# Optimization experiments

Hardware: AMD Instinct MI355X
Metric: run time of the kernel (lower is better)

The kernel has to match this reference:

```python
import jax, jax.numpy as jnp
import numpy as np

N_NODES = 100000
N_REL = 3
N_EDGES = 300000
IN_FEAT = 256
OUT_FEAT = 256


def setup_inputs() -> dict:
    key = jax.random.key(0)
    k1, k2, k3, k4 = jax.random.split(key, 4)
    x = jax.random.normal(k1, (N_NODES, IN_FEAT), dtype=jnp.float32)
    weight = jax.random.normal(k2, (N_REL, IN_FEAT, OUT_FEAT), dtype=jnp.float32)
    src = jax.random.randint(k3, (N_REL, N_EDGES), 0, N_NODES, dtype=jnp.int64)
    dst = jax.random.randint(k4, (N_REL, N_EDGES), 0, N_NODES, dtype=jnp.int64)
    return {"x": x, "weight": weight, "src": src, "dst": dst}


def reference(x, weight, src, dst):
    # Per-relation dense transform: h[r] = x @ W[r]   -> [R, N, out]
    h = jnp.einsum('ni,rio->rno', x, weight)
    n_nodes = x.shape[0]

    # Sparse unweighted-sum aggregation per relation (adj @ h), accumulated
    # into a single destination-node buffer (single node type).
    def agg_one(h_r, src_r, dst_r):
        msgs = h_r[src_r]  # gather source features [E, out]
        return jax.ops.segment_sum(msgs, dst_r, num_segments=n_nodes)

    per_rel = jax.vmap(agg_one)(h, src, dst)  # [R, N, out]
    return jax.nn.relu(per_rel.sum(axis=0))
```

## Files before the change

### kernel.cpp

```cpp
#include <hip/hip_runtime.h>
#include <hip/hip_bf16.h>
#include <stdint.h>

#define M_NODES 100000
#define KF 256
#define NF 256
#define NRELS 3
#define NEDGES 300000
#define TOT_EDGES (NRELS * NEDGES)
#define TOTK (NRELS * M_NODES)
#define KCAT (NRELS * KF)
#define BM 64
#define PAD8 8
#define OVF_SLOTS 16
#define XELEM (M_NODES * KF)
#define EB ((TOT_EDGES + 255) / 256)
#define XCONV_BLOCKS (XELEM / 8 / 256)
#define WT_BLOCKS ((NF * KCAT + 255) / 256)

typedef __attribute__((ext_vector_type(8))) short bf16x8;
typedef __attribute__((ext_vector_type(8))) unsigned short u16x8;
typedef __attribute__((ext_vector_type(4))) float f32x4;

__device__ __forceinline__ unsigned short f32_to_bf16(float f) {
    union { float f; uint32_t u; } c; c.f = f;
    uint32_t u = c.u;
    uint32_t r = (u + 0x7FFFu + ((u >> 16) & 1u)) >> 16;
    return (unsigned short)r;
}

__device__ __forceinline__ float bf16_to_f32(unsigned short s) {
    union { uint32_t u; float f; } c; c.u = ((uint32_t)s) << 16;
    return c.f;
}

__global__ __launch_bounds__(256)
void k_build(const float* __restrict__ x, const float* __restrict__ w,
             const int* __restrict__ src, const int* __restrict__ dst,
             unsigned short* __restrict__ xb, unsigned short* __restrict__ Bt,
             int* __restrict__ counts, int* __restrict__ perm8,
             int* __restrict__ ovf)
{
    int b = blockIdx.x;
    if (b < EB) {
        int e = b * 256 + threadIdx.x;
        if (e < TOT_EDGES) {
            int r = e / NEDGES;
            int key = r * M_NODES + dst[e];
            int pos = atomicAdd(&counts[key], 1);
            if (pos < PAD8)
                perm8[(size_t)key * PAD8 + pos] = src[e];
            else if (pos < PAD8 + OVF_SLOTS)
                ovf[(size_t)key * OVF_SLOTS + (pos - PAD8)] = src[e];
        }
    } else if (b < EB + XCONV_BLOCKS) {
        int gid = (b - EB) * 256 + threadIdx.x;
        const float4* p = (const float4*)x + (size_t)gid * 2;
        float4 u = p[0], v = p[1];
        u16x8 o;
        o[0] = f32_to_bf16(u.x); o[1] = f32_to_bf16(u.y);
        o[2] = f32_to_bf16(u.z); o[3] = f32_to_bf16(u.w);
        o[4] = f32_to_bf16(v.x); o[5] = f32_to_bf16(v.y);
        o[6] = f32_to_bf16(v.z); o[7] = f32_to_bf16(v.w);
        *(u16x8*)(xb + (size_t)gid * 8) = o;
    } else {
        int gid = (b - EB - XCONV_BLOCKS) * 256 + threadIdx.x;
        if (gid < NF * KCAT) {
            int n = gid / KCAT;
            int kc = gid - n * KCAT;
            int r = kc >> 8, k = kc & 255;
            Bt[(size_t)n * KCAT + kc] = f32_to_bf16(w[((size_t)r * KF + k) * NF + n]);
        }
    }
}

__global__ __launch_bounds__(512, 4)
void gemm_ga(const unsigned short* __restrict__ xb,
             const unsigned short* __restrict__ Bt,
             const int* __restrict__ cnt, const int* __restrict__ perm8,
             const int* __restrict__ ovf,
             float* __restrict__ out)
{
    const int d0 = blockIdx.x * BM;
    const int t = threadIdx.x;
    const int lane = t & 63;
    const int wv = t >> 6;
    const int l16 = lane & 15, lg = lane >> 4;
    const int hw = t >> 5;
    const int hl = t & 31;

    __shared__ short As[BM * 256];

    f32x4 acc[4][2] = {};
    const u16x8 zz = (u16x8)0;

    int oc0 = 0, oc1 = 0, oc2 = 0;
    if (hl < 4) {
        int kb = d0 + hw * 4 + hl;
        if (kb >= M_NODES) kb = M_NODES - 1;
        oc0 = cnt[kb];
        oc1 = cnt[M_NODES + kb];
        oc2 = cnt[2 * M_NODES + kb];
    }

    int kpre = d0 + hw * 4 + (hl >> 3);
    if (kpre >= M_NODES) kpre = M_NODES - 1;

    for (int r = 0; r < NRELS; ++r) {
        int ocr = (r == 0) ? oc0 : ((r == 1) ? oc1 : oc2);

        int pv = perm8[((size_t)(r * M_NODES + kpre)) * PAD8 + (hl & 7)];

        if (r) __syncthreads();

#pragma unroll
        for (int q = 0; q < 4; ++q) {
            int n = __shfl(ocr, q, 32);
            if (n > PAD8 + OVF_SLOTS) n = PAD8 + OVF_SLOTS;
            float a0=0.f,a1=0.f,a2=0.f,a3=0.f,a4=0.f,a5=0.f,a6=0.f,a7=0.f;

            auto acc4 = [&](int s0, int s1, int s2, int s3,
                            bool c1, bool c2, bool c3) {
                u16x8 v0 = *(const u16x8*)(xb + (size_t)s0 * KF + hl * 8);
                u16x8 v1 = c1 ? *(const u16x8*)(xb + (size_t)s1 * KF + hl * 8) : zz;
                u16x8 v2 = c2 ? *(const u16x8*)(xb + (size_t)s2 * KF + hl * 8) : zz;
                u16x8 v3 = c3 ? *(const u16x8*)(xb + (size_t)s3 * KF + hl * 8) : zz;
                a0 += bf16_to_f32(v0[0]) + bf16_to_f32(v1[0]) + bf16_to_f32(v2[0]) + bf16_to_f32(v3[0]);
                a1 += bf16_to_f32(v0[1]) + bf16_to_f32(v1[1]) + bf16_to_f32(v2[1]) + bf16_to_f32(v3[1]);
                a2 += bf16_to_f32(v0[2]) + bf16_to_f32(v1[2]) + bf16_to_f32(v2[2]) + bf16_to_f32(v3[2]);
                a3 += bf16_to_f32(v0[3]) + bf16_to_f32(v1[3]) + bf16_to_f32(v2[3]) + bf16_to_f32(v3[3]);
                a4 += bf16_to_f32(v0[4]) + bf16_to_f32(v1[4]) + bf16_to_f32(v2[4]) + bf16_to_f32(v3[4]);
                a5 += bf16_to_f32(v0[5]) + bf16_to_f32(v1[5]) + bf16_to_f32(v2[5]) + bf16_to_f32(v3[5]);
                a6 += bf16_to_f32(v0[6]) + bf16_to_f32(v1[6]) + bf16_to_f32(v2[6]) + bf16_to_f32(v3[6]);
                a7 += bf16_to_f32(v0[7]) + bf16_to_f32(v1[7]) + bf16_to_f32(v2[7]) + bf16_to_f32(v3[7]);
            };

            if (n > 0)
                acc4(__shfl(pv, q * 8 + 0, 32), __shfl(pv, q * 8 + 1, 32),
                     __shfl(pv, q * 8 + 2, 32), __shfl(pv, q * 8 + 3, 32),
                     1 < n, 2 < n, 3 < n);
            if (n > 4)
                acc4(__shfl(pv, q * 8 + 4, 32), __shfl(pv, q * 8 + 5, 32),
                     __shfl(pv, q * 8 + 6, 32), __shfl(pv, q * 8 + 7, 32),
                     5 < n, 6 < n, 7 < n);
            if (n > 8) {
                int kq = d0 + hw * 4 + q;
                if (kq >= M_NODES) kq = M_NODES - 1;
                int ex = (hl < n - 8)
                    ? ovf[((size_t)(r * M_NODES + kq)) * OVF_SLOTS + hl] : 0;
                for (int j = 8; j < n; j += 4) {
                    int s0 = __shfl(ex, j - 8 + 0, 32);
                    int s1 = __shfl(ex, j - 8 + 1, 32);
                    int s2 = __shfl(ex, j - 8 + 2, 32);
                    int s3 = __shfl(ex, j - 8 + 3, 32);
                    acc4(s0, s1, s2, s3, j + 1 < n, j + 2 < n, j + 3 < n);
                }
            }

            int row = hw * 4 + q;
            u16x8 o;
            o[0] = f32_to_bf16(a0); o[1] = f32_to_bf16(a1);
            o[2] = f32_to_bf16(a2); o[3] = f32_to_bf16(a3);
            o[4] = f32_to_bf16(a4); o[5] = f32_to_bf16(a5);
            o[6] = f32_to_bf16(a6); o[7] = f32_to_bf16(a7);
            int slot = hl ^ (row & 7);
            *(u16x8*)((char*)As + row * 512 + slot * 16) = o;
        }
        __syncthreads();

        const unsigned short* bb = Bt + (size_t)(wv * 32 + l16) * KCAT
                                      + r * 256 + lg * 8;
#pragma unroll
        for (int kt = 0; kt < 8; ++kt) {
            bf16x8 bfr[2];
#pragma unroll
            for (int j = 0; j < 2; ++j)
                bfr[j] = *(const bf16x8*)(bb + (size_t)j * 16 * KCAT + kt * 32);
            bf16x8 afr[4];
#pragma unroll
            for (int i = 0; i < 4; ++i) {
                int arow = i * 16 + l16;
                int slot = (kt * 4 + lg) ^ (arow & 7);
                afr[i] = *(bf16x8*)((char*)As + arow * 512 + slot * 16);
            }
#pragma unroll
            for (int i = 0; i < 4; ++i)
#pragma unroll
                for (int j = 0; j < 2; ++j)
                    acc[i][j] = __builtin_amdgcn_mfma_f32_16x16x32_bf16(
                        afr[i], bfr[j], acc[i][j], 0, 0, 0);
        }
    }

#pragma unroll
    for (int i = 0; i < 4; ++i) {
        int row_base = d0 + i * 16 + lg * 4;
#pragma unroll
        for (int q = 0; q < 4; ++q) {
            int row = row_base + q;
            if (row < M_NODES) {
#pragma unroll
                for (int j = 0; j < 2; ++j) {
                    int col = wv * 32 + j * 16 + l16;
                    out[(size_t)row * NF + col] = fmaxf(acc[i][j][q], 0.f);
                }
            }
        }
    }
}

extern "C" void kernel_launch(void* const* d_in, const int* in_sizes, int n_in,
                              void* d_out, int out_size, void* d_ws, size_t ws_size,
                              hipStream_t stream)
{
    const float* x   = (const float*)d_in[0];
    const float* w   = (const float*)d_in[1];
    const int*   src = (const int*)d_in[2];
    const int*   dst = (const int*)d_in[3];
    float* out = (float*)d_out;

    char* ws = (char*)d_ws;
    size_t o = 0;
    int* counts = (int*)(ws + o);  o += (size_t)TOTK * 4;
    int* perm8  = (int*)(ws + o);  o += (size_t)TOTK * PAD8 * 4;
    int* ovf    = (int*)(ws + o);  o += (size_t)TOTK * OVF_SLOTS * 4;
    unsigned short* Bt = (unsigned short*)(ws + o); o += (size_t)NF * KCAT * 2;
    unsigned short* xb = (unsigned short*)(ws + o); o += (size_t)XELEM * 2;

    hipMemsetAsync(counts, 0, (size_t)TOTK * 4, stream);

    k_build<<<EB + XCONV_BLOCKS + WT_BLOCKS, 256, 0, stream>>>(
        x, w, src, dst, xb, Bt, counts, perm8, ovf);

    gemm_ga<<<(M_NODES + BM - 1) / BM, 512, 0, stream>>>(
        xb, Bt, counts, perm8, ovf, out);
}
```

Before: 215.1 us.

## Software-pipeline neighbor gathers across rows and hoist loads above barrier

```diff
diff --git a/kernel.cpp b/kernel.cpp
--- a/kernel.cpp
+++ b/kernel.cpp
@@ -32,6 +32,11 @@
 __device__ __forceinline__ float bf16_to_f32(unsigned short s) {
     union { uint32_t u; float f; } c; c.u = ((uint32_t)s) << 16;
     return c.f;
+}
+
+__device__ __forceinline__ void bar_lgkm() {
+    asm volatile("s_waitcnt lgkmcnt(0)" ::: "memory");
+    __builtin_amdgcn_s_barrier();
 }
 
 __global__ __launch_bounds__(256)
@@ -111,62 +116,77 @@
 
         int pv = perm8[((size_t)(r * M_NODES + kpre)) * PAD8 + (hl & 7)];
 
-        if (r) __syncthreads();
-
-#pragma unroll
-        for (int q = 0; q < 4; ++q) {
-            int n = __shfl(ocr, q, 32);
-            if (n > PAD8 + OVF_SLOTS) n = PAD8 + OVF_SLOTS;
-            float a0=0.f,a1=0.f,a2=0.f,a3=0.f,a4=0.f,a5=0.f,a6=0.f,a7=0.f;
-
-            auto acc4 = [&](int s0, int s1, int s2, int s3,
-                            bool c1, bool c2, bool c3) {
-                u16x8 v0 = *(const u16x8*)(xb + (size_t)s0 * KF + hl * 8);
-                u16x8 v1 = c1 ? *(const u16x8*)(xb + (size_t)s1 * KF + hl * 8) : zz;
-                u16x8 v2 = c2 ? *(const u16x8*)(xb + (size_t)s2 * KF + hl * 8) : zz;
-                u16x8 v3 = c3 ? *(const u16x8*)(xb + (size_t)s3 * KF + hl * 8) : zz;
-                a0 += bf16_to_f32(v0[0]) + bf16_to_f32(v1[0]) + bf16_to_f32(v2[0]) + bf16_to_f32(v3[0]);
-                a1 += bf16_to_f32(v0[1]) + bf16_to_f32(v1[1]) + bf16_to_f32(v2[1]) + bf16_to_f32(v3[1]);
-                a2 += bf16_to_f32(v0[2]) + bf16_to_f32(v1[2]) + bf16_to_f32(v2[2]) + bf16_to_f32(v3[2]);
-                a3 += bf16_to_f32(v0[3]) + bf16_to_f32(v1[3]) + bf16_to_f32(v2[3]) + bf16_to_f32(v3[3]);
-                a4 += bf16_to_f32(v0[4]) + bf16_to_f32(v1[4]) + bf16_to_f32(v2[4]) + bf16_to_f32(v3[4]);
-                a5 += bf16_to_f32(v0[5]) + bf16_to_f32(v1[5]) + bf16_to_f32(v2[5]) + bf16_to_f32(v3[5]);
-                a6 += bf16_to_f32(v0[6]) + bf16_to_f32(v1[6]) + bf16_to_f32(v2[6]) + bf16_to_f32(v3[6]);
-                a7 += bf16_to_f32(v0[7]) + bf16_to_f32(v1[7]) + bf16_to_f32(v2[7]) + bf16_to_f32(v3[7]);
-            };
-
-            if (n > 0)
-                acc4(__shfl(pv, q * 8 + 0, 32), __shfl(pv, q * 8 + 1, 32),
-                     __shfl(pv, q * 8 + 2, 32), __shfl(pv, q * 8 + 3, 32),
-                     1 < n, 2 < n, 3 < n);
-            if (n > 4)
-                acc4(__shfl(pv, q * 8 + 4, 32), __shfl(pv, q * 8 + 5, 32),
-                     __shfl(pv, q * 8 + 6, 32), __shfl(pv, q * 8 + 7, 32),
-                     5 < n, 6 < n, 7 < n);
-            if (n > 8) {
-                int kq = d0 + hw * 4 + q;
-                if (kq >= M_NODES) kq = M_NODES - 1;
-                int ex = (hl < n - 8)
-                    ? ovf[((size_t)(r * M_NODES + kq)) * OVF_SLOTS + hl] : 0;
-                for (int j = 8; j < n; j += 4) {
-                    int s0 = __shfl(ex, j - 8 + 0, 32);
-                    int s1 = __shfl(ex, j - 8 + 1, 32);
-                    int s2 = __shfl(ex, j - 8 + 2, 32);
-                    int s3 = __shfl(ex, j - 8 + 3, 32);
-                    acc4(s0, s1, s2, s3, j + 1 < n, j + 2 < n, j + 3 < n);
-                }
-            }
-
-            int row = hw * 4 + q;
-            u16x8 o;
-            o[0] = f32_to_bf16(a0); o[1] = f32_to_bf16(a1);
-            o[2] = f32_to_bf16(a2); o[3] = f32_to_bf16(a3);
-            o[4] = f32_to_bf16(a4); o[5] = f32_to_bf16(a5);
-            o[6] = f32_to_bf16(a6); o[7] = f32_to_bf16(a7);
-            int slot = hl ^ (row & 7);
-            *(u16x8*)((char*)As + row * 512 + slot * 16) = o;
-        }
-        __syncthreads();
+        int n0 = __shfl(ocr, 0, 32); if (n0 > PAD8 + OVF_SLOTS) n0 = PAD8 + OVF_SLOTS;
+        int n1 = __shfl(ocr, 1, 32); if (n1 > PAD8 + OVF_SLOTS) n1 = PAD8 + OVF_SLOTS;
+        int n2 = __shfl(ocr, 2, 32); if (n2 > PAD8 + OVF_SLOTS) n2 = PAD8 + OVF_SLOTS;
+        int n3 = __shfl(ocr, 3, 32); if (n3 > PAD8 + OVF_SLOTS) n3 = PAD8 + OVF_SLOTS;
+
+        auto LD = [&](int idx) -> u16x8 {
+            int s = __shfl(pv, idx, 32);
+            return *(const u16x8*)(xb + (size_t)s * KF + hl * 8);
+        };
+
+#define LOADA(nn, qq, b0, b1, b2, b3) do {                                     \
+        b0 = zz; b1 = zz; b2 = zz; b3 = zz;                                    \
+        if (nn > 0) b0 = LD((qq) * 8 + 0);                                     \
+        if (nn > 1) b1 = LD((qq) * 8 + 1);                                     \
+        if (nn > 2) b2 = LD((qq) * 8 + 2);                                     \
+        if (nn > 3) b3 = LD((qq) * 8 + 3);                                     \
+    } while (0)
+
+        u16x8 pA0, pA1, pA2, pA3, pB0, pB1, pB2, pB3;
+        LOADA(n0, 0, pA0, pA1, pA2, pA3);
+
+        if (r) bar_lgkm();
+
+#define PROCESS(qq, nn, b0, b1, b2, b3) do {                                   \
+        float a_[8];                                                           \
+        _Pragma("unroll")                                                      \
+        for (int j = 0; j < 8; ++j)                                            \
+            a_[j] = bf16_to_f32(b0[j]) + bf16_to_f32(b1[j])                    \
+                  + bf16_to_f32(b2[j]) + bf16_to_f32(b3[j]);                   \
+        if (nn > 4) {                          \
+            u16x8 t0 = LD((qq) * 8 + 4);                                       \
+            u16x8 t1 = (nn > 5) ? LD((qq) * 8 + 5) : zz;                       \
+            u16x8 t2 = (nn > 6) ? LD((qq) * 8 + 6) : zz;                       \
+            u16x8 t3 = (nn > 7) ? LD((qq) * 8 + 7) : zz;                       \
+            _Pragma("unroll")                                                  \
+            for (int j = 0; j < 8; ++j)                                        \
+                a_[j] += bf16_to_f32(t0[j]) + bf16_to_f32(t1[j])               \
+                       + bf16_to_f32(t2[j]) + bf16_to_f32(t3[j]);              \
+        }                                                                      \
+        if (nn > 8) {                          \
+            int kq = d0 + hw * 4 + (qq);                                       \
+            if (kq >= M_NODES) kq = M_NODES - 1;                               \
+            int ex = (hl < nn - 8)                                             \
+                ? ovf[((size_t)(r * M_NODES + kq)) * OVF_SLOTS + hl] : 0;      \
+            for (int j = 8; j < nn; ++j) {                                     \
+                int s_ = __shfl(ex, j - 8, 32);                                \
+                u16x8 v_ = *(const u16x8*)(xb + (size_t)s_ * KF + hl * 8);     \
+                _Pragma("unroll")                                              \
+                for (int m = 0; m < 8; ++m) a_[m] += bf16_to_f32(v_[m]);       \
+            }                                                                  \
+        }                                                                      \
+        int row_ = hw * 4 + (qq);                                              \
+        u16x8 o_;                                                              \
+        _Pragma("unroll")                                                      \
+        for (int j = 0; j < 8; ++j) o_[j] = f32_to_bf16(a_[j]);                \
+        int slot_ = hl ^ (row_ & 7);                                           \
+        *(u16x8*)((char*)As + row_ * 512 + slot_ * 16) = o_;                   \
+    } while (0)
+
+        LOADA(n1, 1, pB0, pB1, pB2, pB3);
+        PROCESS(0, n0, pA0, pA1, pA2, pA3);
+        LOADA(n2, 2, pA0, pA1, pA2, pA3);
+        PROCESS(1, n1, pB0, pB1, pB2, pB3);
+        LOADA(n3, 3, pB0, pB1, pB2, pB3);
+        PROCESS(2, n2, pA0, pA1, pA2, pA3);
+        PROCESS(3, n3, pB0, pB1, pB2, pB3);
+
+#undef PROCESS
+#undef LOADA
+
+        bar_lgkm();
 
         const unsigned short* bb = Bt + (size_t)(wv * 32 + l16) * KCAT
                                       + r * 256 + lg * 8;
```

After: 231.7 us. 7.7% more time.
